# Kernel optimization log

Hardware: AMD Instinct MI355X
Metric: run time of the kernel (lower is better)

Reference implementation:

```python
import jax, jax.numpy as jnp
import numpy as np

N_QUBITS = 8
BATCH = 65536
PI = float(np.pi)


def rz_mat(t):
    # diag(e^{-i t/2}, e^{+i t/2}); t scalar or [B]
    t = jnp.asarray(t, jnp.float32).astype(jnp.complex64)
    e = jnp.exp(-0.5j * t)
    z = jnp.zeros_like(e)
    return jnp.stack([jnp.stack([e, z], -1), jnp.stack([z, jnp.conj(e)], -1)], -2)


def ry_mat(t):
    t = jnp.asarray(t, jnp.float32)
    c = jnp.cos(0.5 * t).astype(jnp.complex64)
    s = jnp.sin(0.5 * t).astype(jnp.complex64)
    return jnp.stack([jnp.stack([c, -s], -1), jnp.stack([s, c], -1)], -2)


def u3_mat(t, p, l):
    t = jnp.asarray(t, jnp.float32)
    c = jnp.cos(0.5 * t).astype(jnp.complex64)
    s = jnp.sin(0.5 * t).astype(jnp.complex64)
    ep = jnp.exp(1j * jnp.asarray(p, jnp.float32).astype(jnp.complex64))
    el = jnp.exp(1j * jnp.asarray(l, jnp.float32).astype(jnp.complex64))
    return jnp.stack([jnp.stack([c, -el * s], -1), jnp.stack([ep * s, ep * el * c], -1)], -2)


def apply_1q(state, U, w):
    # state: [B] + [2]*N_QUBITS; wire w is axis w+1 (wire 0 most significant, tq convention)
    s = jnp.moveaxis(state, w + 1, -1)
    if U.ndim == 3:  # batched gate (state prep with per-sample angles)
        s = jnp.einsum('b...i,bji->b...j', s, U)
    else:
        s = jnp.einsum('...i,ji->...j', s, U)
    return jnp.moveaxis(s, -1, w + 1)


def apply_cnot(state, c, t):
    s = jnp.moveaxis(state, (c + 1, t + 1), (-2, -1))
    s = jnp.concatenate([s[..., :1, :], s[..., 1:, ::-1]], axis=-2)
    return jnp.moveaxis(s, (-2, -1), (c + 1, t + 1))


def expval_z(state, w):
    p = jnp.square(jnp.abs(state))
    p = jnp.moveaxis(p, w + 1, 1).reshape(p.shape[0], 2, -1).sum(-1)
    return p[:, 0] - p[:, 1]


def build_state(x):
    # circuit_builder substitute: RY(theta), RZ(phi) on every qubit from |0...0>
    B = x.shape[0]
    theta, phi = x[:, 0], x[:, 1]
    state = jnp.zeros((B, 2 ** N_QUBITS), jnp.complex64).at[:, 0].set(1.0)
    state = state.reshape((B,) + (2,) * N_QUBITS)
    Ry, Rz = ry_mat(theta), rz_mat(phi)  # [B,2,2]
    for w in range(N_QUBITS):
        state = apply_1q(state, Ry, w)
        state = apply_1q(state, Rz, w)
    return state


def block(state, a, b, rzp, ry1p, ry2p, fin=None):
    # ZNOTY two-qubit convolution unitary on wires (a, b)
    fin = b if fin is None else fin
    state = apply_1q(state, rz_mat(-PI / 2), a)
    state = apply_cnot(state, a, b)
    state = apply_1q(state, rz_mat(rzp), b)
    state = apply_1q(state, ry_mat(ry1p), a)
    state = apply_cnot(state, b, a)
    state = apply_1q(state, ry_mat(ry2p), a)
    state = apply_cnot(state, a, b)
    state = apply_1q(state, rz_mat(PI / 2), fin)
    return state


def qcnn_forward(x, rz_params, ry_params, u3_params, W1, b1, W2, b2):
    s = build_state(x)
    # conv layer 1 (rz2, rz5, rz8, rz11 -> indices 1,4,7,10)
    s = block(s, 1, 0, rz_params[1], ry_params[0], ry_params[1])
    s = block(s, 3, 2, rz_params[4], ry_params[2], ry_params[3])
    s = block(s, 5, 4, rz_params[7], ry_params[4], ry_params[5])
    s = block(s, 7, 6, rz_params[10], ry_params[6], ry_params[7])
    # (mid-circuit expvals on [0,2,4,6] are non-destructive and discarded -> no state change)
    for i, w in enumerate([1, 3, 5, 7]):
        s = apply_1q(s, u3_mat(u3_params[i, 0], u3_params[i, 1], u3_params[i, 2]), w)
    # conv layer 2 (rz14, rz17, rz20 -> indices 13,16,19); (7,5) block's final fixed RZ
    # lands on wire 1 (as in the original source)
    s = block(s, 3, 1, rz_params[13], ry_params[8], ry_params[9])
    s = block(s, 7, 5, rz_params[16], ry_params[10], ry_params[11], fin=1)
    s = block(s, 5, 3, rz_params[19], ry_params[12], ry_params[13])
    s = apply_1q(s, u3_mat(u3_params[4, 0], u3_params[4, 1], u3_params[4, 2]), 3)
    s = apply_1q(s, u3_mat(u3_params[5, 0], u3_params[5, 1], u3_params[5, 2]), 7)
    feats = jnp.stack([expval_z(s, 3), expval_z(s, 7)], axis=-1)  # [B,2]
    h = jnp.tanh(feats @ W1 + b1)
    return jax.nn.sigmoid(h @ W2 + b2)  # [B,1]


def setup_inputs() -> dict:
    key = jax.random.key(0)
    ks = jax.random.split(key, 8)
    return {
        'x': jax.random.normal(ks[0], (BATCH, 2), jnp.float32),
        'rz_params': jax.random.normal(ks[1], (21,), jnp.float32),
        'ry_params': jax.random.normal(ks[2], (14,), jnp.float32),
        'u3_params': jax.random.normal(ks[3], (6, 3), jnp.float32),
        'W1': jax.random.normal(ks[4], (2, 10), jnp.float32) * 0.5,
        'b1': jax.random.normal(ks[5], (10,), jnp.float32) * 0.1,
        'W2': jax.random.normal(ks[6], (10, 1), jnp.float32) * 0.5,
        'b2': jax.random.normal(ks[7], (1,), jnp.float32) * 0.1,
    }


def reference(x, rz_params, ry_params, u3_params, W1, b1, W2, b2):
    return qcnn_forward(x, rz_params, ry_params, u3_params, W1, b1, W2, b2)
```

## Files before the change

### kernel.cpp

```cpp
#include <hip/hip_runtime.h>
#include <math.h>


__device__ __forceinline__ float2 cmad2(float2 A, float2 a, float2 B, float2 b) {
  return make_float2(A.x*a.x - A.y*a.y + B.x*b.x - B.y*b.y,
                     A.x*a.y + A.y*a.x + B.x*b.y + B.y*b.x);
}

template<int M>
__device__ __forceinline__ void gate1(float2 (&z)[4], int lane,
                                      float2 u00, float2 u01,
                                      float2 u10, float2 u11) {
  if constexpr (M < 64) {
#pragma unroll
    for (int j = 0; j < 4; ++j) {
      float2 pv = make_float2(__shfl_xor(z[j].x, M, 64),
                              __shfl_xor(z[j].y, M, 64));
      bool hi = (lane & M) != 0;
      float2 A = hi ? u11 : u00;
      float2 B = hi ? u10 : u01;
      z[j] = cmad2(A, z[j], B, pv);
    }
  } else {
    constexpr int jb = M >> 6;
#pragma unroll
    for (int j = 0; j < 4; ++j) {
      if ((j & jb) == 0) {
        float2 a = z[j], b = z[j + jb];
        z[j]      = cmad2(u00, a, u01, b);
        z[j + jb] = cmad2(u10, a, u11, b);
      }
    }
  }
}

template<int MC, int MT>
__device__ __forceinline__ void cnotg(float2 (&z)[4], int lane) {
  if constexpr (MT < 64) {
#pragma unroll
    for (int j = 0; j < 4; ++j) {
      bool active = (MC < 64) || (((j << 6) & MC) != 0);
      if (active) {
        float2 pv = make_float2(__shfl_xor(z[j].x, MT, 64),
                                __shfl_xor(z[j].y, MT, 64));
        bool sel = (MC >= 64) || ((lane & MC) != 0);
        z[j].x = sel ? pv.x : z[j].x;
        z[j].y = sel ? pv.y : z[j].y;
      }
    }
  } else {
    constexpr int jb = MT >> 6;
#pragma unroll
    for (int j = 0; j < 4; ++j) {
      if ((j & jb) == 0) {
        if (MC >= 64) {
          constexpr int cjb = MC >> 6;
          if ((j & cjb) != 0) { float2 t = z[j]; z[j] = z[j + jb]; z[j + jb] = t; }
        } else {
          bool sel = (lane & MC) != 0;
          float2 a = z[j], b = z[j + jb];
          z[j]      = make_float2(sel ? b.x : a.x, sel ? b.y : a.y);
          z[j + jb] = make_float2(sel ? a.x : b.x, sel ? a.y : b.y);
        }
      }
    }
  }
}

template<int M>
__device__ __forceinline__ void rzg(float2 (&z)[4], int lane, float t) {
  float s, c; __sincosf(0.5f * t, &s, &c);
  gate1<M>(z, lane, make_float2(c, -s), make_float2(0.f, 0.f),
                    make_float2(0.f, 0.f), make_float2(c, s));
}

template<int M>
__device__ __forceinline__ void ryg(float2 (&z)[4], int lane, float t) {
  float s, c; __sincosf(0.5f * t, &s, &c);
  gate1<M>(z, lane, make_float2(c, 0.f), make_float2(-s, 0.f),
                    make_float2(s, 0.f), make_float2(c, 0.f));
}

template<int M>
__device__ __forceinline__ void u3g(float2 (&z)[4], int lane,
                                    float t, float p, float l) {
  float s, c;  __sincosf(0.5f * t, &s, &c);
  float sp, cp; __sincosf(p, &sp, &cp);
  float sl, cl; __sincosf(l, &sl, &cl);
  float spl, cpl; __sincosf(p + l, &spl, &cpl);
  gate1<M>(z, lane, make_float2(c, 0.f),        make_float2(-cl * s, -sl * s),
                    make_float2(cp * s, sp * s), make_float2(cpl * c, spl * c));
}

template<int MA, int MB, int MF>
__device__ __forceinline__ void blockg(float2 (&z)[4], int lane,
                                       float rzp, float ry1, float ry2) {
  const float Q = 0.70710678118654752f;
  gate1<MA>(z, lane, make_float2(Q, Q), make_float2(0.f, 0.f),
                     make_float2(0.f, 0.f), make_float2(Q, -Q));
  cnotg<MA, MB>(z, lane);
  rzg<MB>(z, lane, rzp);
  ryg<MA>(z, lane, ry1);
  cnotg<MB, MA>(z, lane);
  ryg<MA>(z, lane, ry2);
  cnotg<MA, MB>(z, lane);
  gate1<MF>(z, lane, make_float2(Q, -Q), make_float2(0.f, 0.f),
                     make_float2(0.f, 0.f), make_float2(Q, Q));
}

__device__ __forceinline__ float fast_tanh(float x) {
  float e = __expf(2.f * x);
  return 1.f - 2.f / (e + 1.f);
}

__global__ __launch_bounds__(64)
void qcnn_sim(const float* __restrict__ rz, const float* __restrict__ ry,
              const float* __restrict__ u3, float2* __restrict__ G) {
  int lane = threadIdx.x;
  int p = blockIdx.x;

  float2 z[4];
#pragma unroll
  for (int j = 0; j < 4; ++j) {
    int k = (j << 6) | lane;
    z[j] = make_float2(__popc(k) == p ? 1.f : 0.f, 0.f);
  }

  blockg<2, 1, 1>(z, lane, rz[1],  ry[0],  ry[1]);
  blockg<64, 4, 4>(z, lane, rz[4],  ry[2],  ry[3]);
  blockg<128, 8, 8>(z, lane, rz[7],  ry[4],  ry[5]);
  blockg<32, 16, 16>(z, lane, rz[10], ry[6],  ry[7]);
  u3g<2>(z, lane, u3[0],  u3[1],  u3[2]);
  u3g<64>(z, lane, u3[3],  u3[4],  u3[5]);
  u3g<128>(z, lane, u3[6],  u3[7],  u3[8]);
  u3g<32>(z, lane, u3[9],  u3[10], u3[11]);
  blockg<64, 2, 2>(z, lane, rz[13], ry[8],  ry[9]);
  blockg<32, 128, 2>(z, lane, rz[16], ry[10], ry[11]);
  blockg<128, 64, 64>(z, lane, rz[19], ry[12], ry[13]);
  u3g<64>(z, lane, u3[12], u3[13], u3[14]);
  u3g<32>(z, lane, u3[15], u3[16], u3[17]);

#pragma unroll
  for (int j = 0; j < 4; ++j)
    G[p * 256 + ((j << 6) | lane)] = z[j];
}

__global__ __launch_bounds__(576)
void qcnn_reduce(const float2* __restrict__ G, float4* __restrict__ Stab) {
  int tid = threadIdx.x;
  int wid = tid >> 6, lane = tid & 63;

  float s3 = (lane & 16) ? -1.f : 1.f;
  float s7 = (lane & 8)  ? -1.f : 1.f;

#pragma unroll
  for (int u = 0; u < 5; ++u) {
    int idx = wid * 5 + u;
    int pp = 0, base = 0, s = idx;
    while (s >= base + 9 - pp) { base += 9 - pp; ++pp; }
    int qq = pp + (s - base);

    const float4* rp = (const float4*)(G + pp * 256 + lane * 4);
    const float4* rq = (const float4*)(G + qq * 256 + lane * 4);
    float4 a0 = rp[0], a1 = rp[1];
    float4 b0 = rq[0], b1 = rq[1];

    float SR = a0.x*b0.x + a0.y*b0.y + a0.z*b0.z + a0.w*b0.w
             + a1.x*b1.x + a1.y*b1.y + a1.z*b1.z + a1.w*b1.w;
    float SI = a0.x*b0.y - a0.y*b0.x + a0.z*b0.w - a0.w*b0.z
             + a1.x*b1.y - a1.y*b1.x + a1.z*b1.w - a1.w*b1.z;

    float v0 = s3 * SR, v1 = s3 * SI, v2 = s7 * SR, v3 = s7 * SI;
#pragma unroll
    for (int m = 32; m >= 1; m >>= 1) {
      v0 += __shfl_xor(v0, m, 64);
      v1 += __shfl_xor(v1, m, 64);
      v2 += __shfl_xor(v2, m, 64);
      v3 += __shfl_xor(v3, m, 64);
    }
    if (lane == 0) {
      float sc = (pp == qq) ? 1.f : 2.f;
      Stab[idx] = make_float4(sc * v0, sc * v1, sc * v2, sc * v3);
    }
  }
}

__global__ __launch_bounds__(256)
void qcnn_eval(const float* __restrict__ x, const float4* __restrict__ S,
               const float* __restrict__ W1, const float* __restrict__ b1,
               const float* __restrict__ W2, const float* __restrict__ b2,
               float* __restrict__ out, int B) {
  __shared__ float4 sh[45];
  int tid = threadIdx.x;
  if (tid < 45) sh[tid] = S[tid];
  __syncthreads();

  int i = blockIdx.x * 256 + tid;
  if (i >= B) return;

  float2 tp = reinterpret_cast<const float2*>(x)[i];
  float th = tp.x, ph = tp.y;

  float stt, ct;
  __sincosf(0.5f * th, &stt, &ct);

  float cpw[17], spw[17];
  cpw[0] = 1.f; spw[0] = 1.f;
#pragma unroll
  for (int k = 1; k < 17; ++k) { cpw[k] = cpw[k-1] * ct; spw[k] = spw[k-1] * stt; }

  float cd[9], sd[9];
  cd[0] = 1.f; sd[0] = 0.f;
  __sincosf(ph, &sd[1], &cd[1]);
#pragma unroll
  for (int d = 2; d < 9; ++d) {
    cd[d] = cd[d-1] * cd[1] - sd[d-1] * sd[1];
    sd[d] = sd[d-1] * cd[1] + cd[d-1] * sd[1];
  }

  float f3 = 0.f, f7 = 0.f;
  int sidx = 0;
#pragma unroll
  for (int pp = 0; pp < 9; ++pp) {
#pragma unroll
    for (int qq = pp; qq < 9; ++qq) {
      float4 s4 = sh[sidx]; ++sidx;
      float w = cpw[16 - pp - qq] * spw[pp + qq];
      int d = qq - pp;
      f3 += w * (s4.x * cd[d] - s4.y * sd[d]);
      f7 += w * (s4.z * cd[d] - s4.w * sd[d]);
    }
  }

  float acc = b2[0];
#pragma unroll
  for (int j = 0; j < 10; ++j) {
    float h = fast_tanh(f3 * W1[j] + f7 * W1[10 + j] + b1[j]);
    acc += h * W2[j];
  }
  out[i] = 1.f / (1.f + __expf(-acc));
}

extern "C" void kernel_launch(void* const* d_in, const int* in_sizes, int n_in,
                              void* d_out, int out_size, void* d_ws, size_t ws_size,
                              hipStream_t stream) {
  const float* x  = (const float*)d_in[0];
  const float* rz = (const float*)d_in[1];
  const float* ry = (const float*)d_in[2];
  const float* u3 = (const float*)d_in[3];
  const float* W1 = (const float*)d_in[4];
  const float* b1 = (const float*)d_in[5];
  const float* W2 = (const float*)d_in[6];
  const float* b2 = (const float*)d_in[7];

  float2* G    = (float2*)d_ws;
  float4* Stab = (float4*)((char*)d_ws + 20480);

  qcnn_sim<<<9, 64, 0, stream>>>(rz, ry, u3, G);
  qcnn_reduce<<<1, 576, 0, stream>>>(G, Stab);

  int B = in_sizes[0] / 2;
  qcnn_eval<<<(B + 255) / 256, 256, 0, stream>>>(x, (const float4*)Stab,
                                                 W1, b1, W2, b2,
                                                 (float*)d_out, B);
}
```

Before: 20.61 us.

## Fuse state simulation and reduction into one kernel with DPP lane permutes

Merges the 9-block simulation kernel and the single-block reduction kernel into one 576-thread kernel. The per-sector statevectors now pass through shared memory instead of global memory, which removes one launch and a global round-trip. Cross-lane shuffles use DPP for masks 1, 2 and 8 and ds_bpermute otherwise. Qubits are relabeled onto DPP-friendly lane bits, and RZ/RY gates get specialized cheaper arithmetic. The cost is that the whole precompute runs on a single workgroup.

```diff
diff --git a/kernel.cpp b/kernel.cpp
--- a/kernel.cpp
+++ b/kernel.cpp
@@ -1,37 +1,107 @@
 #include <hip/hip_runtime.h>
 #include <math.h>
 
+
+#define PI_2F 1.57079632679489662f
 
 __device__ __forceinline__ float2 cmad2(float2 A, float2 a, float2 B, float2 b) {
   return make_float2(A.x*a.x - A.y*a.y + B.x*b.x - B.y*b.y,
                      A.x*a.y + A.y*a.x + B.x*b.y + B.y*b.x);
 }
 
-template<int M>
-__device__ __forceinline__ void gate1(float2 (&z)[4], int lane,
-                                      float2 u00, float2 u01,
-                                      float2 u10, float2 u11) {
+template<int CTRL>
+__device__ __forceinline__ float dpps(float v) {
+  int r = __builtin_amdgcn_update_dpp(__float_as_int(v), __float_as_int(v),
+                                      CTRL, 0xF, 0xF, false);
+  return __int_as_float(r);
+}
+
+template<int M>
+__device__ __forceinline__ float lxs(float v, int lane) {
+  if constexpr (M == 1)  return dpps<0xB1>(v);
+  else if constexpr (M == 2) return dpps<0x4E>(v);
+  else if constexpr (M == 8) return dpps<0x128>(v);
+  else {
+    int addr = (lane ^ M) << 2;
+    return __int_as_float(__builtin_amdgcn_ds_bpermute(addr, __float_as_int(v)));
+  }
+}
+
+template<int M>
+__device__ __forceinline__ float2 lx2(float2 v, int lane) {
+  return make_float2(lxs<M>(v.x, lane), lxs<M>(v.y, lane));
+}
+
+template<int M>
+__device__ __forceinline__ void rzd(float2 (&z)[4], int lane, float t) {
+  float s, c; __sincosf(0.5f * t, &s, &c);
+#pragma unroll
+  for (int j = 0; j < 4; ++j) {
+    bool hi;
+    if constexpr (M < 64) hi = (lane & M) != 0;
+    else                  hi = (j & (M >> 6)) != 0;
+    float si = hi ? s : -s;
+    z[j] = make_float2(c * z[j].x - si * z[j].y,
+                       c * z[j].y + si * z[j].x);
+  }
+}
+
+template<int M>
+__device__ __forceinline__ void gate1r(float2 (&z)[4],
+                                       float2 u00, float2 u01,
+                                       float2 u10, float2 u11) {
+  constexpr int jb = M >> 6;
+#pragma unroll
+  for (int j = 0; j < 4; ++j) {
+    if ((j & jb) == 0) {
+      float2 a = z[j], b = z[j + jb];
+      z[j]      = cmad2(u00, a, u01, b);
+      z[j + jb] = cmad2(u10, a, u11, b);
+    }
+  }
+}
+
+template<int M>
+__device__ __forceinline__ void gate1c(float2 (&z)[4], int lane,
+                                       float2 u00, float2 u01,
+                                       float2 u10, float2 u11) {
+  bool hi = (lane & M) != 0;
+  float2 A = hi ? u11 : u00;
+  float2 B = hi ? u10 : u01;
+#pragma unroll
+  for (int j = 0; j < 4; ++j) {
+    float2 pv = lx2<M>(z[j], lane);
+    z[j] = cmad2(A, z[j], B, pv);
+  }
+}
+
+template<int M>
+__device__ __forceinline__ void ryg(float2 (&z)[4], int lane, float t) {
+  float s, c; __sincosf(0.5f * t, &s, &c);
   if constexpr (M < 64) {
+    float sg = (lane & M) ? s : -s;
 #pragma unroll
     for (int j = 0; j < 4; ++j) {
-      float2 pv = make_float2(__shfl_xor(z[j].x, M, 64),
-                              __shfl_xor(z[j].y, M, 64));
-      bool hi = (lane & M) != 0;
-      float2 A = hi ? u11 : u00;
-      float2 B = hi ? u10 : u01;
-      z[j] = cmad2(A, z[j], B, pv);
+      float2 pv = lx2<M>(z[j], lane);
+      z[j] = make_float2(c * z[j].x + sg * pv.x, c * z[j].y + sg * pv.y);
     }
   } else {
-    constexpr int jb = M >> 6;
-#pragma unroll
-    for (int j = 0; j < 4; ++j) {
-      if ((j & jb) == 0) {
-        float2 a = z[j], b = z[j + jb];
-        z[j]      = cmad2(u00, a, u01, b);
-        z[j + jb] = cmad2(u10, a, u11, b);
-      }
-    }
-  }
+    gate1r<M>(z, make_float2(c, 0.f), make_float2(-s, 0.f),
+                 make_float2(s, 0.f), make_float2(c, 0.f));
+  }
+}
+
+template<int M>
+__device__ __forceinline__ void u3g(float2 (&z)[4], int lane,
+                                    float t, float p, float l) {
+  float s, c;  __sincosf(0.5f * t, &s, &c);
+  float sp, cp; __sincosf(p, &sp, &cp);
+  float sl, cl; __sincosf(l, &sl, &cl);
+  float spl, cpl; __sincosf(p + l, &spl, &cpl);
+  float2 u00 = make_float2(c, 0.f),        u01 = make_float2(-cl*s, -sl*s);
+  float2 u10 = make_float2(cp*s, sp*s),    u11 = make_float2(cpl*c, spl*c);
+  if constexpr (M < 64) gate1c<M>(z, lane, u00, u01, u10, u11);
+  else                  gate1r<M>(z, u00, u01, u10, u11);
 }
 
 template<int MC, int MT>
@@ -41,8 +111,7 @@
     for (int j = 0; j < 4; ++j) {
       bool active = (MC < 64) || (((j << 6) & MC) != 0);
       if (active) {
-        float2 pv = make_float2(__shfl_xor(z[j].x, MT, 64),
-                                __shfl_xor(z[j].y, MT, 64));
+        float2 pv = lx2<MT>(z[j], lane);
         bool sel = (MC >= 64) || ((lane & MC) != 0);
         z[j].x = sel ? pv.x : z[j].x;
         z[j].y = sel ? pv.y : z[j].y;
@@ -67,45 +136,17 @@
   }
 }
 
-template<int M>
-__device__ __forceinline__ void rzg(float2 (&z)[4], int lane, float t) {
-  float s, c; __sincosf(0.5f * t, &s, &c);
-  gate1<M>(z, lane, make_float2(c, -s), make_float2(0.f, 0.f),
-                    make_float2(0.f, 0.f), make_float2(c, s));
-}
-
-template<int M>
-__device__ __forceinline__ void ryg(float2 (&z)[4], int lane, float t) {
-  float s, c; __sincosf(0.5f * t, &s, &c);
-  gate1<M>(z, lane, make_float2(c, 0.f), make_float2(-s, 0.f),
-                    make_float2(s, 0.f), make_float2(c, 0.f));
-}
-
-template<int M>
-__device__ __forceinline__ void u3g(float2 (&z)[4], int lane,
-                                    float t, float p, float l) {
-  float s, c;  __sincosf(0.5f * t, &s, &c);
-  float sp, cp; __sincosf(p, &sp, &cp);
-  float sl, cl; __sincosf(l, &sl, &cl);
-  float spl, cpl; __sincosf(p + l, &spl, &cpl);
-  gate1<M>(z, lane, make_float2(c, 0.f),        make_float2(-cl * s, -sl * s),
-                    make_float2(cp * s, sp * s), make_float2(cpl * c, spl * c));
-}
-
 template<int MA, int MB, int MF>
 __device__ __forceinline__ void blockg(float2 (&z)[4], int lane,
                                        float rzp, float ry1, float ry2) {
-  const float Q = 0.70710678118654752f;
-  gate1<MA>(z, lane, make_float2(Q, Q), make_float2(0.f, 0.f),
-                     make_float2(0.f, 0.f), make_float2(Q, -Q));
+  rzd<MA>(z, lane, -PI_2F);
   cnotg<MA, MB>(z, lane);
-  rzg<MB>(z, lane, rzp);
+  rzd<MB>(z, lane, rzp);
   ryg<MA>(z, lane, ry1);
   cnotg<MB, MA>(z, lane);
   ryg<MA>(z, lane, ry2);
   cnotg<MA, MB>(z, lane);
-  gate1<MF>(z, lane, make_float2(Q, -Q), make_float2(0.f, 0.f),
-                     make_float2(0.f, 0.f), make_float2(Q, Q));
+  rzd<MF>(z, lane, PI_2F);
 }
 
 __device__ __forceinline__ float fast_tanh(float x) {
@@ -113,11 +154,24 @@
   return 1.f - 2.f / (e + 1.f);
 }
 
-__global__ __launch_bounds__(64)
-void qcnn_sim(const float* __restrict__ rz, const float* __restrict__ ry,
-              const float* __restrict__ u3, float2* __restrict__ G) {
-  int lane = threadIdx.x;
-  int p = blockIdx.x;
+__device__ __forceinline__ float wsum(float v, int lane) {
+  v += lxs<1>(v, lane);
+  v += lxs<2>(v, lane);
+  v += lxs<4>(v, lane);
+  v += lxs<8>(v, lane);
+  v += lxs<16>(v, lane);
+  v += lxs<32>(v, lane);
+  return v;
+}
+
+#define SSTR 258
+
+__global__ __launch_bounds__(576)
+void qcnn_precompute(const float* __restrict__ rz, const float* __restrict__ ry,
+                     const float* __restrict__ u3, float4* __restrict__ Stab) {
+  __shared__ float2 st[9 * SSTR];
+  int tid = threadIdx.x;
+  int p = tid >> 6, lane = tid & 63;
 
   float2 z[4];
 #pragma unroll
@@ -128,40 +182,35 @@
 
   blockg<2, 1, 1>(z, lane, rz[1],  ry[0],  ry[1]);
   blockg<64, 4, 4>(z, lane, rz[4],  ry[2],  ry[3]);
-  blockg<128, 8, 8>(z, lane, rz[7],  ry[4],  ry[5]);
-  blockg<32, 16, 16>(z, lane, rz[10], ry[6],  ry[7]);
+  blockg<128, 16, 16>(z, lane, rz[7],  ry[4],  ry[5]);
+  blockg<8, 32, 32>(z, lane, rz[10], ry[6],  ry[7]);
   u3g<2>(z, lane, u3[0],  u3[1],  u3[2]);
   u3g<64>(z, lane, u3[3],  u3[4],  u3[5]);
   u3g<128>(z, lane, u3[6],  u3[7],  u3[8]);
-  u3g<32>(z, lane, u3[9],  u3[10], u3[11]);
+  u3g<8>(z, lane, u3[9],  u3[10], u3[11]);
   blockg<64, 2, 2>(z, lane, rz[13], ry[8],  ry[9]);
-  blockg<32, 128, 2>(z, lane, rz[16], ry[10], ry[11]);
+  blockg<8, 128, 2>(z, lane, rz[16], ry[10], ry[11]);
   blockg<128, 64, 64>(z, lane, rz[19], ry[12], ry[13]);
   u3g<64>(z, lane, u3[12], u3[13], u3[14]);
-  u3g<32>(z, lane, u3[15], u3[16], u3[17]);
+  u3g<8>(z, lane, u3[15], u3[16], u3[17]);
 
 #pragma unroll
   for (int j = 0; j < 4; ++j)
-    G[p * 256 + ((j << 6) | lane)] = z[j];
-}
-
-__global__ __launch_bounds__(576)
-void qcnn_reduce(const float2* __restrict__ G, float4* __restrict__ Stab) {
-  int tid = threadIdx.x;
-  int wid = tid >> 6, lane = tid & 63;
+    st[p * SSTR + ((j << 6) | lane)] = z[j];
+  __syncthreads();
 
   float s3 = (lane & 16) ? -1.f : 1.f;
-  float s7 = (lane & 8)  ? -1.f : 1.f;
+  float s7 = (lane & 2)  ? -1.f : 1.f;
 
 #pragma unroll
   for (int u = 0; u < 5; ++u) {
-    int idx = wid * 5 + u;
+    int idx = p * 5 + u;
     int pp = 0, base = 0, s = idx;
     while (s >= base + 9 - pp) { base += 9 - pp; ++pp; }
     int qq = pp + (s - base);
 
-    const float4* rp = (const float4*)(G + pp * 256 + lane * 4);
-    const float4* rq = (const float4*)(G + qq * 256 + lane * 4);
+    const float4* rp = (const float4*)(st + pp * SSTR + lane * 4);
+    const float4* rq = (const float4*)(st + qq * SSTR + lane * 4);
     float4 a0 = rp[0], a1 = rp[1];
     float4 b0 = rq[0], b1 = rq[1];
 
@@ -170,14 +219,11 @@
     float SI = a0.x*b0.y - a0.y*b0.x + a0.z*b0.w - a0.w*b0.z
              + a1.x*b1.y - a1.y*b1.x + a1.z*b1.w - a1.w*b1.z;
 
-    float v0 = s3 * SR, v1 = s3 * SI, v2 = s7 * SR, v3 = s7 * SI;
-#pragma unroll
-    for (int m = 32; m >= 1; m >>= 1) {
-      v0 += __shfl_xor(v0, m, 64);
-      v1 += __shfl_xor(v1, m, 64);
-      v2 += __shfl_xor(v2, m, 64);
-      v3 += __shfl_xor(v3, m, 64);
-    }
+    float v0 = wsum(s3 * SR, lane);
+    float v1 = wsum(s3 * SI, lane);
+    float v2 = wsum(s7 * SR, lane);
+    float v3 = wsum(s7 * SI, lane);
+
     if (lane == 0) {
       float sc = (pp == qq) ? 1.f : 2.f;
       Stab[idx] = make_float4(sc * v0, sc * v1, sc * v2, sc * v3);
@@ -253,11 +299,9 @@
   const float* W2 = (const float*)d_in[6];
   const float* b2 = (const float*)d_in[7];
 
-  float2* G    = (float2*)d_ws;
-  float4* Stab = (float4*)((char*)d_ws + 20480);
-
-  qcnn_sim<<<9, 64, 0, stream>>>(rz, ry, u3, G);
-  qcnn_reduce<<<1, 576, 0, stream>>>(G, Stab);
+  float4* Stab = (float4*)d_ws;
+
+  qcnn_precompute<<<1, 576, 0, stream>>>(rz, ry, u3, Stab);
 
   int B = in_sizes[0] / 2;
   qcnn_eval<<<(B + 255) / 256, 256, 0, stream>>>(x, (const float4*)Stab,
```

After: 22.30 us. 8.2% more time.
